# Performance work log

Measured on AMD Instinct MI355X. Metric: run time of the kernel, lower is better.

The kernel has to match this reference:

```python
import jax, jax.numpy as jnp
import numpy as np

HIDDEN = 64
OUT = 16
NEG = 1e12


def sinusoidal_pos(seq_len, dim, dtype=jnp.float32):
    # kexue.fm SinusoidalPositionEmbedding, merge_mode='zero': [1, S, dim]
    pos = jnp.arange(seq_len, dtype=dtype)[:, None]            # [S,1]
    idx = jnp.arange(dim // 2, dtype=dtype)
    inv_freq = jnp.power(10000.0, -2.0 * idx / dim)            # [dim/2]
    ang = pos * inv_freq[None, :]                              # [S, dim/2]
    emb = jnp.stack([jnp.sin(ang), jnp.cos(ang)], axis=-1)     # [S, dim/2, 2]
    return emb.reshape(seq_len, dim)[None]                     # [1, S, dim]; ::2 = sin, 1::2 = cos


def rotate_half_interleaved(x):
    # result[...,2i] = -x[...,2i+1]; result[...,2i+1] = x[...,2i]
    return jnp.stack([-x[..., 1::2], x[..., ::2]], axis=-1).reshape(x.shape)


def setup_inputs() -> dict:
    key = jax.random.key(0)
    ks = jax.random.split(key, 5)
    B, S, D = 4, 1024, 768
    inputs = jax.random.normal(ks[0], (B, S, D), dtype=jnp.float32)
    mask = jnp.ones((B, S), dtype=jnp.float32)
    W1 = jax.random.normal(ks[1], (D, 2 * HIDDEN), dtype=jnp.float32) * 0.02
    b1 = jax.random.normal(ks[2], (2 * HIDDEN,), dtype=jnp.float32) * 0.02
    W2 = jax.random.normal(ks[3], (2 * HIDDEN, 2 * OUT), dtype=jnp.float32) * 0.02
    b2 = jax.random.normal(ks[4], (2 * OUT,), dtype=jnp.float32) * 0.02
    return {"inputs": inputs, "mask": mask, "W1": W1, "b1": b1, "W2": W2, "b2": b2}


def reference(inputs, mask, W1, b1, W2, b2):
    B, S, _ = inputs.shape
    h = inputs @ W1 + b1                       # [B,S,2H]
    qw, kw = h[..., ::2], h[..., 1::2]         # [B,S,H] each

    pos = sinusoidal_pos(S, HIDDEN, h.dtype)   # [1,S,H]
    cos_pos = jnp.tile(pos[..., 1::2], (1, 1, 2))   # .repeat(1,1,2) tiles, not interleaves
    sin_pos = jnp.tile(pos[..., ::2], (1, 1, 2))
    qw = qw * cos_pos + rotate_half_interleaved(qw) * sin_pos
    kw = kw * cos_pos + rotate_half_interleaved(kw) * sin_pos

    logits = jnp.einsum('bmd,bnd->bmn', qw, kw) / jnp.sqrt(jnp.asarray(HIDDEN, h.dtype))
    bias = jnp.einsum('bnh->bhn', h @ W2 + b2) / 2.0        # [B,2*OUT,S]
    logits = logits[:, None] + bias[:, ::2, None, :] + bias[:, 1::2, :, None]  # [B,OUT,S,S]

    pad = mask[:, None, None, :]                            # broadcast over heads and query dim
    pad = jnp.broadcast_to(pad, (B, OUT, S, S))
    logits = logits * pad - (1.0 - pad) * NEG

    tril = jnp.tril(jnp.ones((S, S), dtype=logits.dtype), -1)
    logits = logits - tril * NEG
    return logits
```

## Files before the change

kernel.cpp:

```cpp
#include <hip/hip_runtime.h>
#include <math.h>

#define NEGV 1000000000000.0f
#define LDSTR 68

__global__ __launch_bounds__(256) void k1_fused(
    const float* __restrict__ x,
    const float* __restrict__ W1,
    const float* __restrict__ b1,
    const float* __restrict__ W2,
    const float* __restrict__ b2,
    float* __restrict__ qw,
    float* __restrict__ kw,
    float* __restrict__ bias)
{
    __shared__ float xs[16][772];
    __shared__ float hs[16][132];
    const int t    = threadIdx.x;
    const int row0 = blockIdx.x * 16;

    {
        const float4* xg = (const float4*)(x + (size_t)row0 * 768);
        #pragma unroll
        for (int it = 0; it < 12; ++it) {
            const int idx = t + it * 256;
            const int r = idx / 192, c4 = idx - r * 192;
            const float4 v = xg[idx];
            *(float4*)&xs[r][c4 * 4] = v;
        }
    }
    __syncthreads();

    const int jc = (t & 31) * 4;
    const int rg = (t >> 5) * 2;
    float accA[4] = {0.f,0.f,0.f,0.f};
    float accB[4] = {0.f,0.f,0.f,0.f};
    #pragma unroll 2
    for (int k = 0; k < 768; k += 4) {
        const float4 xa = *(const float4*)&xs[rg][k];
        const float4 xb = *(const float4*)&xs[rg + 1][k];
        const float xav[4] = {xa.x, xa.y, xa.z, xa.w};
        const float xbv[4] = {xb.x, xb.y, xb.z, xb.w};
        #pragma unroll
        for (int kk = 0; kk < 4; ++kk) {
            const float4 w = *(const float4*)&W1[(size_t)(k + kk) * 128 + jc];
            const float wv[4] = {w.x, w.y, w.z, w.w};
            #pragma unroll
            for (int c = 0; c < 4; ++c) {
                accA[c] = fmaf(xav[kk], wv[c], accA[c]);
                accB[c] = fmaf(xbv[kk], wv[c], accB[c]);
            }
        }
    }
    {
        const float4 bv = *(const float4*)&b1[jc];
        const float bvv[4] = {bv.x, bv.y, bv.z, bv.w};
        #pragma unroll
        for (int c = 0; c < 4; ++c) {
            hs[rg][jc + c]     = accA[c] + bvv[c];
            hs[rg + 1][jc + c] = accB[c] + bvv[c];
        }
    }
    __syncthreads();

    for (int idx = t; idx < 16 * 64; idx += 256) {
        const int r = idx >> 6, c = idx & 63;
        const int rowg = row0 + r;
        const int s = rowg & 1023;
        const int f = c & 31;
        const float invf = exp2f(-0.4152410118609203f * (float)f);
        const float ang = (float)s * invf;
        float sn, cs;
        sincosf(ang, &sn, &cs);
        const int   pc  = (c & 1) ? (c - 1) : (c + 1);
        const float sgn = (c & 1) ? sn : -sn;
        const float qv = fmaf(hs[r][2*c],     cs, hs[r][2*pc]     * sgn);
        const float kv = fmaf(hs[r][2*c + 1], cs, hs[r][2*pc + 1] * sgn);
        qw[(size_t)rowg * 64 + c] = qv;
        kw[(size_t)rowg * 64 + c] = kv;
    }

    for (int idx = t; idx < 16 * 32; idx += 256) {
        const int r = idx >> 5, c = idx & 31;
        const int rowg = row0 + r;
        const int s = rowg & 1023, bb = rowg >> 10;
        float a = 0.f;
        #pragma unroll 4
        for (int k = 0; k < 128; ++k)
            a = fmaf(hs[r][k], W2[k * 32 + c], a);
        bias[(size_t)(bb * 32 + c) * 1024 + s] = (a + b2[c]) * 0.5f;
    }
}

__global__ __launch_bounds__(256) void k2_outer(
    const float* __restrict__ qw, const float* __restrict__ kw,
    const float* __restrict__ bias, const float* __restrict__ mask,
    float* __restrict__ out)
{
    __shared__ float qs[64 * LDSTR];
    __shared__ float ks[64 * LDSTR];
    __shared__ float bA[16][64];
    __shared__ float bB[16][64];
    __shared__ float padv[64];

    const int t  = threadIdx.x;
    const int n0 = blockIdx.x * 64;
    const int m0 = blockIdx.y * 64;
    const int b  = blockIdx.z;

    const float4* qg = (const float4*)(qw + (size_t)(b * 1024 + m0) * 64);
    const float4* kg = (const float4*)(kw + (size_t)(b * 1024 + n0) * 64);
    #pragma unroll
    for (int it = 0; it < 4; ++it) {
        const int idx = t + it * 256;
        const int m = idx >> 4, kgp = idx & 15;
        float4 v = qg[idx];
        qs[(4*kgp + 0) * LDSTR + m] = v.x;
        qs[(4*kgp + 1) * LDSTR + m] = v.y;
        qs[(4*kgp + 2) * LDSTR + m] = v.z;
        qs[(4*kgp + 3) * LDSTR + m] = v.w;
        v = kg[idx];
        ks[(4*kgp + 0) * LDSTR + m] = v.x;
        ks[(4*kgp + 1) * LDSTR + m] = v.y;
        ks[(4*kgp + 2) * LDSTR + m] = v.z;
        ks[(4*kgp + 3) * LDSTR + m] = v.w;
    }
    for (int idx = t; idx < 16 * 64; idx += 256) {
        const int o = idx >> 6, c = idx & 63;
        bA[o][c] = bias[(size_t)(b * 32 + 2*o)     * 1024 + n0 + c];
        bB[o][c] = bias[(size_t)(b * 32 + 2*o + 1) * 1024 + m0 + c];
    }
    if (t < 64) padv[t] = mask[b * 1024 + n0 + t];
    __syncthreads();

    const int tn = t & 15, tm = t >> 4;
    float acc[4][4];
    #pragma unroll
    for (int i = 0; i < 4; ++i)
        #pragma unroll
        for (int c = 0; c < 4; ++c) acc[i][c] = 0.f;

    #pragma unroll 8
    for (int k = 0; k < 64; ++k) {
        const float4 qv = *(const float4*)&qs[k * LDSTR + 4 * tm];
        const float4 kv = *(const float4*)&ks[k * LDSTR + 4 * tn];
        const float qa[4] = {qv.x, qv.y, qv.z, qv.w};
        const float ka[4] = {kv.x, kv.y, kv.z, kv.w};
        #pragma unroll
        for (int i = 0; i < 4; ++i)
            #pragma unroll
            for (int c = 0; c < 4; ++c)
                acc[i][c] = fmaf(qa[i], ka[c], acc[i][c]);
    }

    const float4 pv = *(const float4*)&padv[4 * tn];
    const float p[4] = {pv.x, pv.y, pv.z, pv.w};
    float negterm[4];
    #pragma unroll
    for (int c = 0; c < 4; ++c) negterm[c] = (1.f - p[c]) * NEGV;
    const int ng = n0 + 4 * tn;

    #pragma unroll
    for (int o = 0; o < 16; ++o) {
        const float4 av = *(const float4*)&bA[o][4 * tn];
        const float a[4] = {av.x, av.y, av.z, av.w};
        #pragma unroll
        for (int i = 0; i < 4; ++i) {
            const int mg = m0 + 4 * tm + i;
            const float vb = bB[o][4 * tm + i];
            float rv[4];
            #pragma unroll
            for (int c = 0; c < 4; ++c) {
                float v = fmaf(acc[i][c], 0.125f, a[c] + vb);
                v = v * p[c] - negterm[c];
                if (ng + c < mg) v -= NEGV;
                rv[c] = v;
            }
            float4 r4; r4.x = rv[0]; r4.y = rv[1]; r4.z = rv[2]; r4.w = rv[3];
            *(float4*)(out + ((size_t)((b * 16 + o) * 1024 + mg)) * 1024 + ng) = r4;
        }
    }
}

extern "C" void kernel_launch(void* const* d_in, const int* in_sizes, int n_in,
                              void* d_out, int out_size, void* d_ws, size_t ws_size,
                              hipStream_t stream) {
    const float* x    = (const float*)d_in[0];
    const float* mask = (const float*)d_in[1];
    const float* W1   = (const float*)d_in[2];
    const float* b1   = (const float*)d_in[3];
    const float* W2   = (const float*)d_in[4];
    const float* b2   = (const float*)d_in[5];
    float* out = (float*)d_out;

    float* ws   = (float*)d_ws;
    float* qw   = ws;
    float* kw   = ws + 4096 * 64;
    float* bias = ws + 2 * 4096 * 64;

    hipLaunchKernelGGL(k1_fused, dim3(256), dim3(256), 0, stream,
                       x, W1, b1, W2, b2, qw, kw, bias);
    hipLaunchKernelGGL(k2_outer, dim3(16, 16, 4), dim3(256), 0, stream,
                       qw, kw, bias, mask, out);
}
```

Baseline: 358.5 us.

## Retile outer-product kernel to wide rows and store k transposed

The first kernel splits the W1 reduction across two K halves with 4x4 register tiles and writes kw transposed (feature-major), so the second kernel can load k rows with coalesced float4 and no LDS transpose. The outer kernel now uses 16x256 tiles where each wavefront writes 1 KB contiguous row segments. It also fuses the mask and causal terms into precomputed per-element constants so each output is two FMAs. This targets store efficiency on the write-bound 256 MB output, at the cost of an extra LDS reduction and sync in the first kernel and more total k traffic in the second.

```diff
diff --git a/kernel.cpp b/kernel.cpp
--- a/kernel.cpp
+++ b/kernel.cpp
@@ -2,7 +2,6 @@
 #include <math.h>
 
 #define NEGV 1000000000000.0f
-#define LDSTR 68
 
 __global__ __launch_bounds__(256) void k1_fused(
     const float* __restrict__ x,
@@ -11,11 +10,11 @@
     const float* __restrict__ W2,
     const float* __restrict__ b2,
     float* __restrict__ qw,
-    float* __restrict__ kw,
+    float* __restrict__ kwt,
     float* __restrict__ bias)
 {
     __shared__ float xs[16][772];
-    __shared__ float hs[16][132];
+    __shared__ float hs[2][16][132];
     const int t    = threadIdx.x;
     const int row0 = blockIdx.x * 16;
 
@@ -31,42 +30,63 @@
     }
     __syncthreads();
 
-    const int jc = (t & 31) * 4;
-    const int rg = (t >> 5) * 2;
-    float accA[4] = {0.f,0.f,0.f,0.f};
-    float accB[4] = {0.f,0.f,0.f,0.f};
-    #pragma unroll 2
-    for (int k = 0; k < 768; k += 4) {
-        const float4 xa = *(const float4*)&xs[rg][k];
-        const float4 xb = *(const float4*)&xs[rg + 1][k];
-        const float xav[4] = {xa.x, xa.y, xa.z, xa.w};
-        const float xbv[4] = {xb.x, xb.y, xb.z, xb.w};
-        #pragma unroll
-        for (int kk = 0; kk < 4; ++kk) {
-            const float4 w = *(const float4*)&W1[(size_t)(k + kk) * 128 + jc];
-            const float wv[4] = {w.x, w.y, w.z, w.w};
-            #pragma unroll
-            for (int c = 0; c < 4; ++c) {
-                accA[c] = fmaf(xav[kk], wv[c], accA[c]);
-                accB[c] = fmaf(xbv[kk], wv[c], accB[c]);
+    {
+        const int jc = (t & 31) * 4;
+        const int rg = ((t >> 5) & 3) * 4;
+        const int kh = t >> 7;
+        const int k0 = kh * 384;
+
+        float acc[4][4] = {{0.f, 0.f, 0.f, 0.f}};
+        #pragma unroll 2
+        for (int k = 0; k < 384; k += 4) {
+            const float4 xv0 = *(const float4*)&xs[rg + 0][k0 + k];
+            const float4 xv1 = *(const float4*)&xs[rg + 1][k0 + k];
+            const float4 xv2 = *(const float4*)&xs[rg + 2][k0 + k];
+            const float4 xv3 = *(const float4*)&xs[rg + 3][k0 + k];
+            const float xa[4][4] = {
+                {xv0.x, xv0.y, xv0.z, xv0.w},
+                {xv1.x, xv1.y, xv1.z, xv1.w},
+                {xv2.x, xv2.y, xv2.z, xv2.w},
+                {xv3.x, xv3.y, xv3.z, xv3.w}};
+            #pragma unroll
+            for (int kk = 0; kk < 4; ++kk) {
+                const float4 w = *(const float4*)&W1[(size_t)(k0 + k + kk) * 128 + jc];
+                const float wv[4] = {w.x, w.y, w.z, w.w};
+                #pragma unroll
+                for (int i = 0; i < 4; ++i) {
+                    #pragma unroll
+                    for (int c = 0; c < 4; ++c)
+                        acc[i][c] = fmaf(xa[i][kk], wv[c], acc[i][c]);
+                }
             }
         }
-    }
-    {
         const float4 bv = *(const float4*)&b1[jc];
         const float bvv[4] = {bv.x, bv.y, bv.z, bv.w};
         #pragma unroll
-        for (int c = 0; c < 4; ++c) {
-            hs[rg][jc + c]     = accA[c] + bvv[c];
-            hs[rg + 1][jc + c] = accB[c] + bvv[c];
+        for (int i = 0; i < 4; ++i) {
+            float4 hv;
+            hv.x = acc[i][0] + (kh == 0 ? bvv[0] : 0.f);
+            hv.y = acc[i][1] + (kh == 0 ? bvv[1] : 0.f);
+            hv.z = acc[i][2] + (kh == 0 ? bvv[2] : 0.f);
+            hv.w = acc[i][3] + (kh == 0 ? bvv[3] : 0.f);
+            *(float4*)&hs[kh][rg + i][jc] = hv;
         }
     }
     __syncthreads();
 
-    for (int idx = t; idx < 16 * 64; idx += 256) {
-        const int r = idx >> 6, c = idx & 63;
-        const int rowg = row0 + r;
-        const int s = rowg & 1023;
+    #pragma unroll
+    for (int it = 0; it < 8; ++it) {
+        const int idx = t + it * 256;
+        const int r = idx >> 7, c = idx & 127;
+        hs[0][r][c] += hs[1][r][c];
+    }
+    __syncthreads();
+
+    #pragma unroll
+    for (int it = 0; it < 4; ++it) {
+        const int idx = t + it * 256;
+        const int c = idx & 63, r = idx >> 6;
+        const int s = (row0 + r) & 1023;
         const int f = c & 31;
         const float invf = exp2f(-0.4152410118609203f * (float)f);
         const float ang = (float)s * invf;
@@ -74,110 +94,138 @@
         sincosf(ang, &sn, &cs);
         const int   pc  = (c & 1) ? (c - 1) : (c + 1);
         const float sgn = (c & 1) ? sn : -sn;
-        const float qv = fmaf(hs[r][2*c],     cs, hs[r][2*pc]     * sgn);
-        const float kv = fmaf(hs[r][2*c + 1], cs, hs[r][2*pc + 1] * sgn);
-        qw[(size_t)rowg * 64 + c] = qv;
-        kw[(size_t)rowg * 64 + c] = kv;
-    }
-
-    for (int idx = t; idx < 16 * 32; idx += 256) {
-        const int r = idx >> 5, c = idx & 31;
-        const int rowg = row0 + r;
-        const int s = rowg & 1023, bb = rowg >> 10;
-        float a = 0.f;
-        #pragma unroll 4
-        for (int k = 0; k < 128; ++k)
-            a = fmaf(hs[r][k], W2[k * 32 + c], a);
-        bias[(size_t)(bb * 32 + c) * 1024 + s] = (a + b2[c]) * 0.5f;
+        const float qv = fmaf(hs[0][r][2 * c], cs, hs[0][r][2 * pc] * sgn);
+        qw[(size_t)(row0 + r) * 64 + c] = qv;
+    }
+
+    #pragma unroll
+    for (int it = 0; it < 4; ++it) {
+        const int idx = t + it * 256;
+        const int mi = idx & 15, c = idx >> 4;
+        const int s = (row0 + mi) & 1023;
+        const int f = c & 31;
+        const float invf = exp2f(-0.4152410118609203f * (float)f);
+        const float ang = (float)s * invf;
+        float sn, cs;
+        sincosf(ang, &sn, &cs);
+        const int   pc  = (c & 1) ? (c - 1) : (c + 1);
+        const float sgn = (c & 1) ? sn : -sn;
+        const float kv = fmaf(hs[0][mi][2 * c + 1], cs, hs[0][mi][2 * pc + 1] * sgn);
+        kwt[(size_t)c * 4096 + row0 + mi] = kv;
+    }
+
+    {
+        const int s0 = row0 & 1023, bb = row0 >> 10;
+        #pragma unroll
+        for (int it = 0; it < 2; ++it) {
+            const int idx = t + it * 256;
+            const int mi = idx & 15, c = idx >> 4;
+            float a = 0.f;
+            #pragma unroll 4
+            for (int k = 0; k < 128; ++k)
+                a = fmaf(hs[0][mi][k], W2[k * 32 + c], a);
+            bias[(size_t)(bb * 32 + c) * 1024 + s0 + mi] = (a + b2[c]) * 0.5f;
+        }
     }
 }
 
-__global__ __launch_bounds__(256) void k2_outer(
-    const float* __restrict__ qw, const float* __restrict__ kw,
-    const float* __restrict__ bias, const float* __restrict__ mask,
+__global__ __launch_bounds__(256, 4) void k2_outer(
+    const float* __restrict__ qw,
+    const float* __restrict__ kwt,
+    const float* __restrict__ bias,
+    const float* __restrict__ mask,
     float* __restrict__ out)
 {
-    __shared__ float qs[64 * LDSTR];
-    __shared__ float ks[64 * LDSTR];
-    __shared__ float bA[16][64];
-    __shared__ float bB[16][64];
-    __shared__ float padv[64];
+    __shared__ float ks[32][260];
+    __shared__ float qs[16][68];
+    __shared__ float bBs[16][16];
 
     const int t  = threadIdx.x;
-    const int n0 = blockIdx.x * 64;
-    const int m0 = blockIdx.y * 64;
+    const int n0 = blockIdx.x * 256;
+    const int m0 = blockIdx.y * 16;
     const int b  = blockIdx.z;
-
-    const float4* qg = (const float4*)(qw + (size_t)(b * 1024 + m0) * 64);
-    const float4* kg = (const float4*)(kw + (size_t)(b * 1024 + n0) * 64);
-    #pragma unroll
-    for (int it = 0; it < 4; ++it) {
-        const int idx = t + it * 256;
-        const int m = idx >> 4, kgp = idx & 15;
-        float4 v = qg[idx];
-        qs[(4*kgp + 0) * LDSTR + m] = v.x;
-        qs[(4*kgp + 1) * LDSTR + m] = v.y;
-        qs[(4*kgp + 2) * LDSTR + m] = v.z;
-        qs[(4*kgp + 3) * LDSTR + m] = v.w;
-        v = kg[idx];
-        ks[(4*kgp + 0) * LDSTR + m] = v.x;
-        ks[(4*kgp + 1) * LDSTR + m] = v.y;
-        ks[(4*kgp + 2) * LDSTR + m] = v.z;
-        ks[(4*kgp + 3) * LDSTR + m] = v.w;
-    }
-    for (int idx = t; idx < 16 * 64; idx += 256) {
-        const int o = idx >> 6, c = idx & 63;
-        bA[o][c] = bias[(size_t)(b * 32 + 2*o)     * 1024 + n0 + c];
-        bB[o][c] = bias[(size_t)(b * 32 + 2*o + 1) * 1024 + m0 + c];
-    }
-    if (t < 64) padv[t] = mask[b * 1024 + n0 + t];
-    __syncthreads();
-
-    const int tn = t & 15, tm = t >> 4;
-    float acc[4][4];
-    #pragma unroll
-    for (int i = 0; i < 4; ++i)
-        #pragma unroll
-        for (int c = 0; c < 4; ++c) acc[i][c] = 0.f;
-
-    #pragma unroll 8
-    for (int k = 0; k < 64; ++k) {
-        const float4 qv = *(const float4*)&qs[k * LDSTR + 4 * tm];
-        const float4 kv = *(const float4*)&ks[k * LDSTR + 4 * tn];
-        const float qa[4] = {qv.x, qv.y, qv.z, qv.w};
-        const float ka[4] = {kv.x, kv.y, kv.z, kv.w};
-        #pragma unroll
-        for (int i = 0; i < 4; ++i)
-            #pragma unroll
-            for (int c = 0; c < 4; ++c)
-                acc[i][c] = fmaf(qa[i], ka[c], acc[i][c]);
-    }
-
-    const float4 pv = *(const float4*)&padv[4 * tn];
+    const int L  = t & 63;
+    const int w  = t >> 6;
+
+    {
+        const int r = t >> 4, kq = t & 15;
+        *(float4*)&qs[r][kq * 4] =
+            *(const float4*)&qw[(size_t)(b * 1024 + m0 + r) * 64 + kq * 4];
+        bBs[r][kq] = bias[(size_t)(b * 32 + 2 * r + 1) * 1024 + m0 + kq];
+    }
+
+    float acc[4][4] = {{0.f, 0.f, 0.f, 0.f}};
+    for (int kc = 0; kc < 2; ++kc) {
+        if (kc) __syncthreads();
+        {
+            const float4* kg4 = (const float4*)kwt;
+            const int col4 = (b * 1024 + n0) >> 2;
+            #pragma unroll
+            for (int it = 0; it < 8; ++it) {
+                const int idx = t + it * 256;
+                const int kk = idx >> 6, nq = idx & 63;
+                const float4 v = kg4[(size_t)(kc * 32 + kk) * 1024 + col4 + nq];
+                *(float4*)&ks[kk][nq * 4] = v;
+            }
+        }
+        __syncthreads();
+
+        #pragma unroll
+        for (int kg = 0; kg < 8; ++kg) {
+            float4 kv[4];
+            #pragma unroll
+            for (int kk = 0; kk < 4; ++kk)
+                kv[kk] = *(const float4*)&ks[kg * 4 + kk][4 * L];
+            const float4 q0 = *(const float4*)&qs[4 * w + 0][kc * 32 + kg * 4];
+            const float4 q1 = *(const float4*)&qs[4 * w + 1][kc * 32 + kg * 4];
+            const float4 q2 = *(const float4*)&qs[4 * w + 2][kc * 32 + kg * 4];
+            const float4 q3 = *(const float4*)&qs[4 * w + 3][kc * 32 + kg * 4];
+            const float qa[4][4] = {
+                {q0.x, q0.y, q0.z, q0.w},
+                {q1.x, q1.y, q1.z, q1.w},
+                {q2.x, q2.y, q2.z, q2.w},
+                {q3.x, q3.y, q3.z, q3.w}};
+            #pragma unroll
+            for (int kk = 0; kk < 4; ++kk) {
+                const float kvv[4] = {kv[kk].x, kv[kk].y, kv[kk].z, kv[kk].w};
+                #pragma unroll
+                for (int i = 0; i < 4; ++i) {
+                    #pragma unroll
+                    for (int c = 0; c < 4; ++c)
+                        acc[i][c] = fmaf(qa[i][kk], kvv[c], acc[i][c]);
+                }
+            }
+        }
+    }
+
+    const float4 pv = *(const float4*)&mask[b * 1024 + n0 + 4 * L];
     const float p[4] = {pv.x, pv.y, pv.z, pv.w};
-    float negterm[4];
-    #pragma unroll
-    for (int c = 0; c < 4; ++c) negterm[c] = (1.f - p[c]) * NEGV;
-    const int ng = n0 + 4 * tn;
-
-    #pragma unroll
+    float mneg[4][4];
+    #pragma unroll
+    for (int i = 0; i < 4; ++i) {
+        const int mg = m0 + 4 * w + i;
+        #pragma unroll
+        for (int c = 0; c < 4; ++c) {
+            float wsub = (1.f - p[c]) * NEGV;
+            if (n0 + 4 * L + c < mg) wsub += NEGV;
+            mneg[i][c] = -wsub;
+        }
+    }
+    float* outb = out + (size_t)b * 16 * 1024 * 1024 + n0 + 4 * L;
+    #pragma unroll 2
     for (int o = 0; o < 16; ++o) {
-        const float4 av = *(const float4*)&bA[o][4 * tn];
+        const float4 av = *(const float4*)&bias[(size_t)(b * 32 + 2 * o) * 1024 + n0 + 4 * L];
         const float a[4] = {av.x, av.y, av.z, av.w};
         #pragma unroll
         for (int i = 0; i < 4; ++i) {
-            const int mg = m0 + 4 * tm + i;
-            const float vb = bB[o][4 * tm + i];
-            float rv[4];
-            #pragma unroll
-            for (int c = 0; c < 4; ++c) {
-                float v = fmaf(acc[i][c], 0.125f, a[c] + vb);
-                v = v * p[c] - negterm[c];
-                if (ng + c < mg) v -= NEGV;
-                rv[c] = v;
-            }
-            float4 r4; r4.x = rv[0]; r4.y = rv[1]; r4.z = rv[2]; r4.w = rv[3];
-            *(float4*)(out + ((size_t)((b * 16 + o) * 1024 + mg)) * 1024 + ng) = r4;
+            const int mg = m0 + 4 * w + i;
+            const float vb = bBs[o][4 * w + i];
+            float4 r4;
+            r4.x = fmaf(fmaf(acc[i][0], 0.125f, a[0] + vb), p[0], mneg[i][0]);
+            r4.y = fmaf(fmaf(acc[i][1], 0.125f, a[1] + vb), p[1], mneg[i][1]);
+            r4.z = fmaf(fmaf(acc[i][2], 0.125f, a[2] + vb), p[2], mneg[i][2]);
+            r4.w = fmaf(fmaf(acc[i][3], 0.125f, a[3] + vb), p[3], mneg[i][3]);
+            *(float4*)&outb[(size_t)(o * 1024 + mg) * 1024] = r4;
         }
     }
 }
@@ -195,11 +243,11 @@
 
     float* ws   = (float*)d_ws;
     float* qw   = ws;
-    float* kw   = ws + 4096 * 64;
+    float* kwt  = ws + 4096 * 64;
     float* bias = ws + 2 * 4096 * 64;
 
     hipLaunchKernelGGL(k1_fused, dim3(256), dim3(256), 0, stream,
-                       x, W1, b1, W2, b2, qw, kw, bias);
-    hipLaunchKernelGGL(k2_outer, dim3(16, 16, 4), dim3(256), 0, stream,
-                       qw, kw, bias, mask, out);
+                       x, W1, b1, W2, b2, qw, kwt, bias);
+    hipLaunchKernelGGL(k2_outer, dim3(4, 64, 4), dim3(256), 0, stream,
+                       qw, kwt, bias, mask, out);
 }
```

Result: slower. 370.8 us (+3.4%).

## Split QK matmul from head broadcast into separate kernels via workspace

Applied to the files above, without the earlier changes.

The fused outer kernel is split in two. One kernel computes the scaled QK^T logits into a [B,S,S] workspace buffer. A second kernel reads that buffer and broadcasts it across the 16 heads with bias, mask and causal terms, each thread writing full 4 KB rows with float4 stores. The aim is better write coalescing and occupancy for the dominant 268 MB output store. The cost is an extra 16 MB write and 2x-reread of intermediate plus one more launch.

```diff
diff --git a/kernel.cpp b/kernel.cpp
--- a/kernel.cpp
+++ b/kernel.cpp
@@ -92,16 +92,12 @@
     }
 }
 
-__global__ __launch_bounds__(256) void k2_outer(
+__global__ __launch_bounds__(256) void k2a_qk(
     const float* __restrict__ qw, const float* __restrict__ kw,
-    const float* __restrict__ bias, const float* __restrict__ mask,
-    float* __restrict__ out)
+    float* __restrict__ qk8)
 {
     __shared__ float qs[64 * LDSTR];
     __shared__ float ks[64 * LDSTR];
-    __shared__ float bA[16][64];
-    __shared__ float bB[16][64];
-    __shared__ float padv[64];
 
     const int t  = threadIdx.x;
     const int n0 = blockIdx.x * 64;
@@ -125,12 +121,6 @@
         ks[(4*kgp + 2) * LDSTR + m] = v.z;
         ks[(4*kgp + 3) * LDSTR + m] = v.w;
     }
-    for (int idx = t; idx < 16 * 64; idx += 256) {
-        const int o = idx >> 6, c = idx & 63;
-        bA[o][c] = bias[(size_t)(b * 32 + 2*o)     * 1024 + n0 + c];
-        bB[o][c] = bias[(size_t)(b * 32 + 2*o + 1) * 1024 + m0 + c];
-    }
-    if (t < 64) padv[t] = mask[b * 1024 + n0 + t];
     __syncthreads();
 
     const int tn = t & 15, tm = t >> 4;
@@ -153,32 +143,75 @@
                 acc[i][c] = fmaf(qa[i], ka[c], acc[i][c]);
     }
 
-    const float4 pv = *(const float4*)&padv[4 * tn];
+    const int ng = n0 + 4 * tn;
+    #pragma unroll
+    for (int i = 0; i < 4; ++i) {
+        const int mg = m0 + 4 * tm + i;
+        float4 r4;
+        r4.x = acc[i][0] * 0.125f;
+        r4.y = acc[i][1] * 0.125f;
+        r4.z = acc[i][2] * 0.125f;
+        r4.w = acc[i][3] * 0.125f;
+        *(float4*)(qk8 + ((size_t)(b * 1024 + mg)) * 1024 + ng) = r4;
+    }
+}
+
+__global__ __launch_bounds__(256) void k2b_bcast(
+    const float* __restrict__ qk8,
+    const float* __restrict__ bias,
+    const float* __restrict__ mask,
+    float* __restrict__ out)
+{
+    const int t  = threadIdx.x;
+    const int o1 = blockIdx.x;
+    const int m0 = blockIdx.y * 8;
+    const int b  = blockIdx.z;
+    const int n  = 4 * t;
+
+    const float4 pv = *(const float4*)&mask[b * 1024 + n];
     const float p[4] = {pv.x, pv.y, pv.z, pv.w};
-    float negterm[4];
-    #pragma unroll
-    for (int c = 0; c < 4; ++c) negterm[c] = (1.f - p[c]) * NEGV;
-    const int ng = n0 + 4 * tn;
-
-    #pragma unroll
-    for (int o = 0; o < 16; ++o) {
-        const float4 av = *(const float4*)&bA[o][4 * tn];
+
+    float Q[2][4];
+    float vb[2][8];
+    #pragma unroll
+    for (int s = 0; s < 2; ++s) {
+        const int o = o1 + 8 * s;
+        const float4 av = *(const float4*)&bias[(size_t)(b * 32 + 2 * o) * 1024 + n];
         const float a[4] = {av.x, av.y, av.z, av.w};
         #pragma unroll
-        for (int i = 0; i < 4; ++i) {
-            const int mg = m0 + 4 * tm + i;
-            const float vb = bB[o][4 * tm + i];
-            float rv[4];
-            #pragma unroll
-            for (int c = 0; c < 4; ++c) {
-                float v = fmaf(acc[i][c], 0.125f, a[c] + vb);
-                v = v * p[c] - negterm[c];
-                if (ng + c < mg) v -= NEGV;
-                rv[c] = v;
-            }
-            float4 r4; r4.x = rv[0]; r4.y = rv[1]; r4.z = rv[2]; r4.w = rv[3];
-            *(float4*)(out + ((size_t)((b * 16 + o) * 1024 + mg)) * 1024 + ng) = r4;
-        }
+        for (int c = 0; c < 4; ++c)
+            Q[s][c] = a[c] * p[c] - (1.f - p[c]) * NEGV;
+        const float4 v0 = *(const float4*)&bias[(size_t)(b * 32 + 2 * o + 1) * 1024 + m0];
+        const float4 v1 = *(const float4*)&bias[(size_t)(b * 32 + 2 * o + 1) * 1024 + m0 + 4];
+        vb[s][0] = v0.x; vb[s][1] = v0.y; vb[s][2] = v0.z; vb[s][3] = v0.w;
+        vb[s][4] = v1.x; vb[s][5] = v1.y; vb[s][6] = v1.z; vb[s][7] = v1.w;
+    }
+
+    const float* qrow = qk8 + ((size_t)(b * 1024 + m0)) * 1024 + n;
+    float* ob0 = out + ((size_t)((b * 16 + o1)     * 1024 + m0)) * 1024 + n;
+    float* ob1 = out + ((size_t)((b * 16 + o1 + 8) * 1024 + m0)) * 1024 + n;
+
+    #pragma unroll
+    for (int r = 0; r < 8; ++r) {
+        const int m = m0 + r;
+        const float4 qv = *(const float4*)&qrow[(size_t)r * 1024];
+        const float q[4] = {qv.x, qv.y, qv.z, qv.w};
+        float cz[4];
+        #pragma unroll
+        for (int c = 0; c < 4; ++c)
+            cz[c] = (n + c < m) ? NEGV : 0.f;
+
+        float4 r0, r1;
+        r0.x = fmaf(q[0] + vb[0][r], p[0], Q[0][0]) - cz[0];
+        r0.y = fmaf(q[1] + vb[0][r], p[1], Q[0][1]) - cz[1];
+        r0.z = fmaf(q[2] + vb[0][r], p[2], Q[0][2]) - cz[2];
+        r0.w = fmaf(q[3] + vb[0][r], p[3], Q[0][3]) - cz[3];
+        r1.x = fmaf(q[0] + vb[1][r], p[0], Q[1][0]) - cz[0];
+        r1.y = fmaf(q[1] + vb[1][r], p[1], Q[1][1]) - cz[1];
+        r1.z = fmaf(q[2] + vb[1][r], p[2], Q[1][2]) - cz[2];
+        r1.w = fmaf(q[3] + vb[1][r], p[3], Q[1][3]) - cz[3];
+        *(float4*)&ob0[(size_t)r * 1024] = r0;
+        *(float4*)&ob1[(size_t)r * 1024] = r1;
     }
 }
 
@@ -197,9 +230,12 @@
     float* qw   = ws;
     float* kw   = ws + 4096 * 64;
     float* bias = ws + 2 * 4096 * 64;
+    float* qk8  = ws + 2 * 4096 * 64 + 4 * 32 * 1024;
 
     hipLaunchKernelGGL(k1_fused, dim3(256), dim3(256), 0, stream,
                        x, W1, b1, W2, b2, qw, kw, bias);
-    hipLaunchKernelGGL(k2_outer, dim3(16, 16, 4), dim3(256), 0, stream,
-                       qw, kw, bias, mask, out);
-}
+    hipLaunchKernelGGL(k2a_qk, dim3(16, 16, 4), dim3(256), 0, stream,
+                       qw, kw, qk8);
+    hipLaunchKernelGGL(k2b_bcast, dim3(8, 128, 4), dim3(256), 0, stream,
+                       qk8, bias, mask, out);
+}
```

Result: slower. 375.9 us (+4.8%).
